# Performance work log

Measured on AMD Instinct MI355X. Metric: run time of the kernel, lower is better.

Reference implementation:

```python
import jax, jax.numpy as jnp
import numpy as np

N = 50000
E = 800000
IN_DIM = 128
LABEL_DIM = 32
D_MODEL = 128
REL_DIM = 32
NUM_LABELS = 1000
REL_BUCKETS = 1024
N_LAYERS = 2
EPS = 1e-5


def setup_inputs() -> dict:
    key = jax.random.key(0)
    ks = jax.random.split(key, 16)
    s = 0.02
    return {
        "x": jax.random.normal(ks[0], (N, IN_DIM), jnp.float32),
        "label": jax.random.randint(ks[1], (N,), 0, NUM_LABELS),
        "edge_index": jax.random.randint(ks[2], (2, E), 0, N),
        "edge_rel": jax.random.randint(ks[3], (E,), 0, REL_BUCKETS),
        "label_emb": jax.random.normal(ks[4], (NUM_LABELS, LABEL_DIM), jnp.float32) * s,
        "in_proj_w": jax.random.normal(ks[5], (IN_DIM + LABEL_DIM, D_MODEL), jnp.float32) * s,
        "in_proj_b": jnp.zeros((D_MODEL,), jnp.float32),
        "rel_emb": jax.random.normal(ks[6], (N_LAYERS, REL_BUCKETS, REL_DIM), jnp.float32) * s,
        "lin_neigh_w": jax.random.normal(ks[7], (N_LAYERS, D_MODEL, D_MODEL), jnp.float32) * s,
        "lin_self_w": jax.random.normal(ks[8], (N_LAYERS, D_MODEL, D_MODEL), jnp.float32) * s,
        "lin_self_b": jnp.zeros((N_LAYERS, D_MODEL), jnp.float32),
        "lin_rel_w": jax.random.normal(ks[9], (N_LAYERS, REL_DIM, D_MODEL), jnp.float32) * s,
        "ln_g": jnp.ones((N_LAYERS, D_MODEL), jnp.float32),
        "ln_b": jnp.zeros((N_LAYERS, D_MODEL), jnp.float32),
    }


def _layernorm(x, g, b):
    mu = jnp.mean(x, axis=-1, keepdims=True)
    var = jnp.mean(jnp.square(x - mu), axis=-1, keepdims=True)
    return (x - mu) * jax.lax.rsqrt(var + EPS) * g + b


def reference(x, label, edge_index, edge_rel, label_emb, in_proj_w, in_proj_b,
              rel_emb, lin_neigh_w, lin_self_w, lin_self_b, lin_rel_w, ln_g, ln_b):
    n = x.shape[0]
    src, dst = edge_index[0], edge_index[1]
    # input projection
    h = jnp.concatenate([x, label_emb[label]], axis=-1) @ in_proj_w + in_proj_b
    h = jax.nn.relu(h)
    # in-degree for mean aggregation (PyG 'mean' gives 0 for isolated nodes)
    deg = jax.ops.segment_sum(jnp.ones((src.shape[0],), h.dtype), dst, num_segments=n)
    inv_deg = jnp.where(deg > 0, 1.0 / jnp.maximum(deg, 1.0), 0.0)[:, None]
    for l in range(N_LAYERS):
        rel = rel_emb[l][edge_rel]                                   # [E, rel_dim]
        msg = h[src] @ lin_neigh_w[l] + rel @ lin_rel_w[l]           # [E, d]
        agg = jax.ops.segment_sum(msg, dst, num_segments=n) * inv_deg
        out = h @ lin_self_w[l] + lin_self_b[l] + agg
        h = _layernorm(jax.nn.relu(out), ln_g[l], ln_b[l])
    return h
```

## Files before the change

### kernel.cpp

```cpp
#include <hip/hip_runtime.h>
#include <hip/hip_bf16.h>

#define N_NODES 50000
#define N_EDGES 800000
#define D 128
#define LABEL_DIM 32
#define REL_DIM 32
#define REL_BUCKETS 1024
#define NUM_LABELS 1000
#define LN_EPS 1e-5f

#define NB 196
#define CAP 6144
#define EPB 1024
#define NE_BLOCKS 782

#define PB_IN 80
#define PB_LEMB 125
#define PB_CAT 144
#define PB_REL 32
#define PREP_UNITS (PB_IN + PB_LEMB + 2 * PB_CAT + 2 * PB_REL)

#define BSTR 144

typedef short bf16x8 __attribute__((ext_vector_type(8)));
typedef float f32x4 __attribute__((ext_vector_type(4)));
typedef float f32x2 __attribute__((ext_vector_type(2)));
typedef unsigned int u32x2 __attribute__((ext_vector_type(2)));
typedef unsigned int u32x4 __attribute__((ext_vector_type(4)));

__device__ inline unsigned short f2bf(float f) {
    __hip_bfloat16 h = __float2bfloat16(f);
    return *reinterpret_cast<unsigned short*>(&h);
}
__device__ inline float bf2f(unsigned short u) {
    return __uint_as_float((unsigned)u << 16);
}

__device__ inline void pack8_fp8(const bf16x8 bv, unsigned& lo, unsigned& hi) {
    float f0 = bf2f((unsigned short)bv[0]), f1 = bf2f((unsigned short)bv[1]);
    float f2 = bf2f((unsigned short)bv[2]), f3 = bf2f((unsigned short)bv[3]);
    float f4 = bf2f((unsigned short)bv[4]), f5 = bf2f((unsigned short)bv[5]);
    float f6 = bf2f((unsigned short)bv[6]), f7 = bf2f((unsigned short)bv[7]);
    lo = __builtin_amdgcn_cvt_pk_fp8_f32(f0, f1, 0u, false);
    lo = __builtin_amdgcn_cvt_pk_fp8_f32(f2, f3, lo, true);
    hi = __builtin_amdgcn_cvt_pk_fp8_f32(f4, f5, 0u, false);
    hi = __builtin_amdgcn_cvt_pk_fp8_f32(f6, f7, hi, true);
}

__global__ __launch_bounds__(256) void scatter_prep_kernel(
    const int* __restrict__ src, const int* __restrict__ dst, const int* __restrict__ rel,
    int* __restrict__ gcur, unsigned* __restrict__ staged_pk, unsigned char* __restrict__ staged_dl,
    const float* __restrict__ in_proj_w, const float* __restrict__ label_emb,
    const float* __restrict__ lin_neigh_w, const float* __restrict__ lin_self_w,
    const float* __restrict__ lin_rel_w, const float* __restrict__ rel_emb,
    unsigned short* __restrict__ Btx, unsigned short* __restrict__ leb,
    unsigned short* __restrict__ Btc0, unsigned short* __restrict__ Btc1,
    unsigned short* __restrict__ relb0, unsigned short* __restrict__ relb1) {
    __shared__ int hist[NB];
    __shared__ int lcur[NB];
    const int t = threadIdx.x;
    const int bid = blockIdx.x;

    if (bid >= NE_BLOCKS) {
        int u = bid - NE_BLOCKS;
        if (u < PB_IN) {
            int idx = u * 256 + t;
            int n = idx / 160, k = idx % 160;
            Btx[idx] = f2bf(in_proj_w[k * 128 + n]);
            return;
        }
        u -= PB_IN;
        if (u < PB_LEMB) {
            int i = u * 256 + t;
            if (i < NUM_LABELS * LABEL_DIM) leb[i] = f2bf(label_emb[i]);
            return;
        }
        u -= PB_LEMB;
        if (u < 2 * PB_CAT) {
            int l = u >= PB_CAT;
            int cb = l ? u - PB_CAT : u;
            int idx = cb * 256 + t;
            int n = idx / 288, k = idx % 288;
            const float* Ws = lin_self_w + (size_t)l * 128 * 128;
            const float* Wn = lin_neigh_w + (size_t)l * 128 * 128;
            const float* Wr = lin_rel_w + (size_t)l * REL_DIM * 128;
            float v = (k < 128) ? Ws[(size_t)k * 128 + n]
                    : (k < 256) ? Wn[(size_t)(k - 128) * 128 + n]
                                : Wr[(size_t)(k - 256) * 128 + n];
            (l ? Btc1 : Btc0)[idx] = f2bf(v);
            return;
        }
        u -= 2 * PB_CAT;
        {
            int l = u >= PB_REL;
            int rb = l ? u - PB_REL : u;
            int idx = rb * 1024 + t * 4;
            float4 v = *(const float4*)(rel_emb + (size_t)l * REL_BUCKETS * REL_DIM + idx);
            unsigned short* out = (l ? relb1 : relb0) + idx;
            out[0] = f2bf(v.x); out[1] = f2bf(v.y);
            out[2] = f2bf(v.z); out[3] = f2bf(v.w);
            return;
        }
    }

    for (int i = t; i < NB; i += 256) hist[i] = 0;
    __syncthreads();
    const int e0 = bid * EPB;
    unsigned char bb[4], dl[4];
#pragma unroll
    for (int i = 0; i < 4; ++i) {
        int e = e0 + i * 256 + t;
        if (e < N_EDGES) {
            int d = dst[e];
            bb[i] = (unsigned char)(d >> 8);
            dl[i] = (unsigned char)(d & 255);
            atomicAdd(&hist[d >> 8], 1);
        }
    }
    __syncthreads();
    for (int b = t; b < NB; b += 256) {
        int hc = hist[b];
        lcur[b] = hc ? (b * CAP + atomicAdd(&gcur[b], hc)) : 0;
    }
    __syncthreads();
#pragma unroll
    for (int i = 0; i < 4; ++i) {
        int e = e0 + i * 256 + t;
        if (e < N_EDGES) {
            int pos = atomicAdd(&lcur[bb[i]], 1);
            staged_pk[pos] = (unsigned)src[e] | ((unsigned)rel[e] << 16);
            staged_dl[pos] = dl[i];
        }
    }
}

__global__ __launch_bounds__(256) void place_in_kernel(
    const int* __restrict__ gcur,
    const unsigned* __restrict__ staged_pk, const unsigned char* __restrict__ staged_dl,
    int* __restrict__ off, int* __restrict__ deg, unsigned* __restrict__ csr_pk,
    const float* __restrict__ X, const unsigned short* __restrict__ Btx,
    const unsigned short* __restrict__ leb, const int* __restrict__ label,
    const float* __restrict__ bias, unsigned short* __restrict__ hb,
    unsigned char* __restrict__ hb8) {
    __shared__ __align__(16) char smem[128 * 160 * 2];
    const int t = threadIdx.x;
    const int bid = blockIdx.x;

    if (bid < NB) {
        int* ph = (int*)smem;
        int* pbuf = ph + 256;
        int* pcur = pbuf + 256;
        const int beg = bid * CAP;
        const int end = beg + gcur[bid];
        ph[t] = 0;
        __syncthreads();
        for (int i = beg + t; i < end; i += 256) atomicAdd(&ph[staged_dl[i]], 1);
        __syncthreads();
        int v = ph[t];
        pbuf[t] = v;
        __syncthreads();
        for (int o = 1; o < 256; o <<= 1) {
            int tv = (t >= o) ? pbuf[t - o] : 0;
            __syncthreads();
            pbuf[t] += tv;
            __syncthreads();
        }
        int node_off = beg + pbuf[t] - v;
        int node = bid * 256 + t;
        if (node < N_NODES) {
            off[node] = node_off;
            deg[node] = v;
        }
        pcur[t] = node_off;
        __syncthreads();
        for (int i = beg + t; i < end; i += 256) {
            int pos = atomicAdd(&pcur[staged_dl[i]], 1);
            csr_pk[pos] = staged_pk[i];
        }
        return;
    }

    unsigned short* sB = (unsigned short*)smem;
    const int mb = bid - NB;
#pragma unroll
    for (int i = 0; i < 10; ++i) {
        int c = t + i * 256;
        int col = c / 20, kch = c % 20;
        int dstc = col * 20 + (kch < 16 ? (kch ^ (col & 7)) : kch);
        *(bf16x8*)&sB[dstc * 8] = *(const bf16x8*)&Btx[c * 8];
    }
    __syncthreads();

    const int wave = t >> 6, lane = t & 63;
    const int m16 = lane & 15, q = lane >> 4;
    const int r0 = mb * 64 + wave * 16;
    const int arow = r0 + m16;
    const bool avalid = arow < N_NODES;
    const float* xp = X + (size_t)(avalid ? arow : 0) * 128 + q * 8;

    f32x4 acc[8];
#pragma unroll
    for (int ct = 0; ct < 8; ++ct) acc[ct] = (f32x4){0.f, 0.f, 0.f, 0.f};

#pragma unroll
    for (int ki = 0; ki < 4; ++ki) {
        bf16x8 af;
        if (avalid) {
            float4 v0 = *(const float4*)(xp + ki * 32);
            float4 v1 = *(const float4*)(xp + ki * 32 + 4);
            af[0] = (short)f2bf(v0.x); af[1] = (short)f2bf(v0.y);
            af[2] = (short)f2bf(v0.z); af[3] = (short)f2bf(v0.w);
            af[4] = (short)f2bf(v1.x); af[5] = (short)f2bf(v1.y);
            af[6] = (short)f2bf(v1.z); af[7] = (short)f2bf(v1.w);
        } else {
            af = (bf16x8){0, 0, 0, 0, 0, 0, 0, 0};
        }
        int kch = ki * 4 + q;
#pragma unroll
        for (int ct = 0; ct < 8; ++ct) {
            int col = ct * 16 + m16;
            int chunk = col * 20 + (kch ^ (m16 & 7));
            bf16x8 bf = *(const bf16x8*)&sB[chunk * 8];
            acc[ct] = __builtin_amdgcn_mfma_f32_16x16x32_bf16(af, bf, acc[ct], 0, 0, 0);
        }
    }
    {
        int lb = avalid ? label[arow] : 0;
        bf16x8 af = *(const bf16x8*)(leb + (size_t)lb * LABEL_DIM + q * 8);
        if (!avalid) af = (bf16x8){0, 0, 0, 0, 0, 0, 0, 0};
        int kch = 16 + q;
#pragma unroll
        for (int ct = 0; ct < 8; ++ct) {
            int col = ct * 16 + m16;
            int chunk = col * 20 + kch;
            bf16x8 bf = *(const bf16x8*)&sB[chunk * 8];
            acc[ct] = __builtin_amdgcn_mfma_f32_16x16x32_bf16(af, bf, acc[ct], 0, 0, 0);
        }
    }

    unsigned short hbv[8][4];
#pragma unroll
    for (int ct = 0; ct < 8; ++ct) {
        int colg = ct * 16 + m16;
        float bs = bias[colg];
#pragma unroll
        for (int r = 0; r < 4; ++r) {
            int row = r0 + q * 4 + r;
            float v = fmaxf(acc[ct][r] + bs, 0.f);
            hbv[ct][r] = f2bf(v);
            if (row < N_NODES) hb[(size_t)row * 128 + colg] = hbv[ct][r];
        }
    }

    __syncthreads();
    unsigned short* bounce = sB;
#pragma unroll
    for (int ct = 0; ct < 8; ++ct) {
        int colg = ct * 16 + m16;
#pragma unroll
        for (int r = 0; r < 4; ++r)
            bounce[(wave * 16 + q * 4 + r) * BSTR + colg] = hbv[ct][r];
    }
    __syncthreads();
    {
        int rl = t >> 2;
        int grow = mb * 64 + rl;
        if (grow < N_NODES) {
            const unsigned short* bp = bounce + rl * BSTR + (t & 3) * 32;
            unsigned o[8];
#pragma unroll
            for (int k = 0; k < 4; ++k) {
                bf16x8 bv = *(const bf16x8*)(bp + k * 8);
                pack8_fp8(bv, o[2 * k], o[2 * k + 1]);
            }
            u32x4* dp = (u32x4*)(hb8 + (size_t)grow * 128 + (t & 3) * 32);
            dp[0] = (u32x4){o[0], o[1], o[2], o[3]};
            dp[1] = (u32x4){o[4], o[5], o[6], o[7]};
        }
    }
}

__global__ __launch_bounds__(256) void agg_raw_kernel(const unsigned char* __restrict__ hb8,
                                                      const unsigned short* __restrict__ relb,
                                                      const int* __restrict__ off,
                                                      const int* __restrict__ deg,
                                                      const unsigned* __restrict__ csr_pk,
                                                      unsigned short* __restrict__ Sm,
                                                      unsigned short* __restrict__ Rm) {
    const int wave = threadIdx.x >> 6;
    const int lane = threadIdx.x & 63;
    const int node = blockIdx.x * 4 + wave;
    if (node >= N_NODES) return;
    const int q = lane >> 4, l16 = lane & 15;
    const int beg = off[node];
    const int dcnt = deg[node];
    const int co = l16 * 8;

    float acc[8];
    float ra0 = 0.f, ra1 = 0.f;
#pragma unroll
    for (int j = 0; j < 8; ++j) acc[j] = 0.f;

    unsigned pkv = 0;
    if (lane < dcnt) pkv = csr_pk[beg + lane];

    const int dcl = dcnt < 64 ? dcnt : 64;
    for (int s = 0; s < dcl; s += 16) {
        unsigned pkk[4];
        float mk[4];
#pragma unroll
        for (int k = 0; k < 4; ++k) {
            int slot = s + k * 4 + q;
            pkk[k] = (unsigned)__shfl((int)pkv, slot);
            mk[k] = (slot < dcnt) ? 1.f : 0.f;
        }
#pragma unroll
        for (int k = 0; k < 4; ++k) {
            u32x2 hv = *(const u32x2*)(hb8 + ((size_t)(pkk[k] & 0xffffu) << 7) + co);
            unsigned rw = *(const unsigned*)(relb + ((size_t)(pkk[k] >> 16) << 5) + l16 * 2);
            float m = mk[k];
            f32x2 d0 = __builtin_amdgcn_cvt_pk_f32_fp8(hv[0], false);
            f32x2 d1 = __builtin_amdgcn_cvt_pk_f32_fp8(hv[0], true);
            f32x2 d2 = __builtin_amdgcn_cvt_pk_f32_fp8(hv[1], false);
            f32x2 d3 = __builtin_amdgcn_cvt_pk_f32_fp8(hv[1], true);
            acc[0] = fmaf(m, d0[0], acc[0]); acc[1] = fmaf(m, d0[1], acc[1]);
            acc[2] = fmaf(m, d1[0], acc[2]); acc[3] = fmaf(m, d1[1], acc[3]);
            acc[4] = fmaf(m, d2[0], acc[4]); acc[5] = fmaf(m, d2[1], acc[5]);
            acc[6] = fmaf(m, d3[0], acc[6]); acc[7] = fmaf(m, d3[1], acc[7]);
            ra0 = fmaf(m, bf2f((unsigned short)(rw & 0xffffu)), ra0);
            ra1 = fmaf(m, bf2f((unsigned short)(rw >> 16)), ra1);
        }
    }

    const int end = beg + dcnt;
    for (int e = beg + 64; e < end; e += 8) {
        int i0 = e + q, i1 = e + 4 + q;
        float m0 = 1.f, m1 = 1.f;
        if (i0 >= end) { i0 = beg; m0 = 0.f; }
        if (i1 >= end) { i1 = beg; m1 = 0.f; }
        unsigned pk0 = csr_pk[i0];
        unsigned pk1 = csr_pk[i1];
        u32x2 hv0 = *(const u32x2*)(hb8 + ((size_t)(pk0 & 0xffffu) << 7) + co);
        u32x2 hv1 = *(const u32x2*)(hb8 + ((size_t)(pk1 & 0xffffu) << 7) + co);
        unsigned rw0 = *(const unsigned*)(relb + ((size_t)(pk0 >> 16) << 5) + l16 * 2);
        unsigned rw1 = *(const unsigned*)(relb + ((size_t)(pk1 >> 16) << 5) + l16 * 2);
        {
            f32x2 d0 = __builtin_amdgcn_cvt_pk_f32_fp8(hv0[0], false);
            f32x2 d1 = __builtin_amdgcn_cvt_pk_f32_fp8(hv0[0], true);
            f32x2 d2 = __builtin_amdgcn_cvt_pk_f32_fp8(hv0[1], false);
            f32x2 d3 = __builtin_amdgcn_cvt_pk_f32_fp8(hv0[1], true);
            acc[0] = fmaf(m0, d0[0], acc[0]); acc[1] = fmaf(m0, d0[1], acc[1]);
            acc[2] = fmaf(m0, d1[0], acc[2]); acc[3] = fmaf(m0, d1[1], acc[3]);
            acc[4] = fmaf(m0, d2[0], acc[4]); acc[5] = fmaf(m0, d2[1], acc[5]);
            acc[6] = fmaf(m0, d3[0], acc[6]); acc[7] = fmaf(m0, d3[1], acc[7]);
        }
        {
            f32x2 d0 = __builtin_amdgcn_cvt_pk_f32_fp8(hv1[0], false);
            f32x2 d1 = __builtin_amdgcn_cvt_pk_f32_fp8(hv1[0], true);
            f32x2 d2 = __builtin_amdgcn_cvt_pk_f32_fp8(hv1[1], false);
            f32x2 d3 = __builtin_amdgcn_cvt_pk_f32_fp8(hv1[1], true);
            acc[0] = fmaf(m1, d0[0], acc[0]); acc[1] = fmaf(m1, d0[1], acc[1]);
            acc[2] = fmaf(m1, d1[0], acc[2]); acc[3] = fmaf(m1, d1[1], acc[3]);
            acc[4] = fmaf(m1, d2[0], acc[4]); acc[5] = fmaf(m1, d2[1], acc[5]);
            acc[6] = fmaf(m1, d3[0], acc[6]); acc[7] = fmaf(m1, d3[1], acc[7]);
        }
        ra0 = fmaf(m0, bf2f((unsigned short)(rw0 & 0xffffu)), ra0);
        ra1 = fmaf(m0, bf2f((unsigned short)(rw0 >> 16)), ra1);
        ra0 = fmaf(m1, bf2f((unsigned short)(rw1 & 0xffffu)), ra0);
        ra1 = fmaf(m1, bf2f((unsigned short)(rw1 >> 16)), ra1);
    }

#pragma unroll
    for (int j = 0; j < 8; ++j) {
        acc[j] += __shfl_xor(acc[j], 16);
        acc[j] += __shfl_xor(acc[j], 32);
    }
    ra0 += __shfl_xor(ra0, 16); ra0 += __shfl_xor(ra0, 32);
    ra1 += __shfl_xor(ra1, 16); ra1 += __shfl_xor(ra1, 32);

    float inv = (dcnt > 0) ? 1.f / (float)dcnt : 0.f;
    if (q == 0) {
        bf16x8 ob;
#pragma unroll
        for (int j = 0; j < 8; ++j) ob[j] = (short)f2bf(acc[j] * inv);
        *(bf16x8*)(Sm + ((size_t)node << 7) + co) = ob;
        unsigned pk = (unsigned)f2bf(ra0 * inv) | ((unsigned)f2bf(ra1 * inv) << 16);
        ((unsigned*)(Rm + ((size_t)node << 5)))[l16] = pk;
    }
}

template <bool LAST>
__global__ __launch_bounds__(256) void gemm_ln_kernel(const unsigned short* __restrict__ Btc,
                                                      unsigned short* __restrict__ hb,
                                                      unsigned char* __restrict__ hb8,
                                                      const unsigned short* __restrict__ Sm,
                                                      const unsigned short* __restrict__ Rm,
                                                      const float* __restrict__ bias,
                                                      const float* __restrict__ g,
                                                      const float* __restrict__ b,
                                                      float* __restrict__ hout) {
    __shared__ unsigned short sB[128 * 36 * 8];
    const int t = threadIdx.x;
#pragma unroll
    for (int i = 0; i < 18; ++i) {
        int c = t + i * 256;
        int col = c / 36, kch = c % 36;
        int swz = (kch < 32) ? (kch ^ (col & 7)) : (32 + ((kch - 32) ^ (col & 3)));
        *(bf16x8*)&sB[(col * 36 + swz) * 8] = *(const bf16x8*)&Btc[c * 8];
    }
    __syncthreads();

    const int wave = t >> 6, lane = t & 63;
    const int m16 = lane & 15, q = lane >> 4;
    const int r0 = blockIdx.x * 64 + wave * 16;
    const int arow = r0 + m16;
    const bool avalid = arow < N_NODES;
    const int sr = avalid ? arow : 0;
    const unsigned short* hp = hb + (size_t)sr * 128 + q * 8;
    const unsigned short* sp = Sm + (size_t)sr * 128 + q * 8;
    const unsigned short* rp = Rm + (size_t)sr * 32 + q * 8;

    f32x4 acc[8];
#pragma unroll
    for (int ct = 0; ct < 8; ++ct) acc[ct] = (f32x4){0.f, 0.f, 0.f, 0.f};
    const bf16x8 zf = (bf16x8){0, 0, 0, 0, 0, 0, 0, 0};

#pragma unroll
    for (int ki = 0; ki < 4; ++ki) {
        bf16x8 af = *(const bf16x8*)(hp + ki * 32);
        if (!avalid) af = zf;
        int kch = ki * 4 + q;
#pragma unroll
        for (int ct = 0; ct < 8; ++ct) {
            int col = ct * 16 + m16;
            bf16x8 bf = *(const bf16x8*)&sB[(col * 36 + (kch ^ (m16 & 7))) * 8];
            acc[ct] = __builtin_amdgcn_mfma_f32_16x16x32_bf16(af, bf, acc[ct], 0, 0, 0);
        }
    }
#pragma unroll
    for (int ki = 0; ki < 4; ++ki) {
        bf16x8 af = *(const bf16x8*)(sp + ki * 32);
        if (!avalid) af = zf;
        int kch = 16 + ki * 4 + q;
#pragma unroll
        for (int ct = 0; ct < 8; ++ct) {
            int col = ct * 16 + m16;
            bf16x8 bf = *(const bf16x8*)&sB[(col * 36 + (kch ^ (m16 & 7))) * 8];
            acc[ct] = __builtin_amdgcn_mfma_f32_16x16x32_bf16(af, bf, acc[ct], 0, 0, 0);
        }
    }
    {
        bf16x8 af = *(const bf16x8*)rp;
        if (!avalid) af = zf;
#pragma unroll
        for (int ct = 0; ct < 8; ++ct) {
            int col = ct * 16 + m16;
            bf16x8 bf = *(const bf16x8*)&sB[(col * 36 + 32 + (q ^ (m16 & 3))) * 8];
            acc[ct] = __builtin_amdgcn_mfma_f32_16x16x32_bf16(af, bf, acc[ct], 0, 0, 0);
        }
    }

    float bs[8], gs[8], bbs[8];
#pragma unroll
    for (int ct = 0; ct < 8; ++ct) {
        int cg2 = ct * 16 + m16;
        bs[ct] = bias[cg2];
        gs[ct] = g[cg2];
        bbs[ct] = b[cg2];
    }
    unsigned short hbv[4][8];
#pragma unroll
    for (int r = 0; r < 4; ++r) {
        int row = r0 + q * 4 + r;
        float v[8];
        float s = 0.f;
#pragma unroll
        for (int ct = 0; ct < 8; ++ct) {
            float val = fmaxf(acc[ct][r] + bs[ct], 0.f);
            v[ct] = val;
            s += val;
        }
#pragma unroll
        for (int o = 8; o > 0; o >>= 1) s += __shfl_xor(s, o);
        float mu = s * (1.f / 128.f);
        float qs = 0.f;
#pragma unroll
        for (int ct = 0; ct < 8; ++ct) {
            float dd = v[ct] - mu;
            v[ct] = dd;
            qs += dd * dd;
        }
#pragma unroll
        for (int o = 8; o > 0; o >>= 1) qs += __shfl_xor(qs, o);
        float rstd = rsqrtf(qs * (1.f / 128.f) + LN_EPS);
#pragma unroll
        for (int ct = 0; ct < 8; ++ct) {
            int colg = ct * 16 + m16;
            float o2 = v[ct] * rstd * gs[ct] + bbs[ct];
            hbv[r][ct] = f2bf(o2);
            if (row < N_NODES) {
                if constexpr (LAST) {
                    hout[(size_t)row * 128 + colg] = o2;
                } else {
                    hb[(size_t)row * 128 + colg] = hbv[r][ct];
                }
            }
        }
    }

    if constexpr (!LAST) {
        __syncthreads();
        unsigned short* bounce = sB;
#pragma unroll
        for (int r = 0; r < 4; ++r) {
            int rl = wave * 16 + q * 4 + r;
#pragma unroll
            for (int ct = 0; ct < 8; ++ct)
                bounce[rl * BSTR + ct * 16 + m16] = hbv[r][ct];
        }
        __syncthreads();
        int rl = t >> 2;
        int grow = blockIdx.x * 64 + rl;
        if (grow < N_NODES) {
            const unsigned short* bp = bounce + rl * BSTR + (t & 3) * 32;
            unsigned o[8];
#pragma unroll
            for (int k = 0; k < 4; ++k) {
                bf16x8 bv = *(const bf16x8*)(bp + k * 8);
                pack8_fp8(bv, o[2 * k], o[2 * k + 1]);
            }
            u32x4* dp = (u32x4*)(hb8 + (size_t)grow * 128 + (t & 3) * 32);
            dp[0] = (u32x4){o[0], o[1], o[2], o[3]};
            dp[1] = (u32x4){o[4], o[5], o[6], o[7]};
        }
    }
}


extern "C" void kernel_launch(void* const* d_in, const int* in_sizes, int n_in,
                              void* d_out, int out_size, void* d_ws, size_t ws_size,
                              hipStream_t stream) {
    const float* x          = (const float*)d_in[0];
    const int*   label      = (const int*)d_in[1];
    const int*   edge_index = (const int*)d_in[2];
    const int*   edge_rel   = (const int*)d_in[3];
    const float* label_emb  = (const float*)d_in[4];
    const float* in_proj_w  = (const float*)d_in[5];
    const float* in_proj_b  = (const float*)d_in[6];
    const float* rel_emb    = (const float*)d_in[7];
    const float* lin_neigh_w = (const float*)d_in[8];
    const float* lin_self_w  = (const float*)d_in[9];
    const float* lin_self_b  = (const float*)d_in[10];
    const float* lin_rel_w   = (const float*)d_in[11];
    const float* ln_g        = (const float*)d_in[12];
    const float* ln_b        = (const float*)d_in[13];
    float* h = (float*)d_out;

    char* p = (char*)d_ws;
    auto alloc = [&](size_t bytes) {
        char* r = p;
        p += (bytes + 255) & ~(size_t)255;
        return r;
    };
    int* gcur        = (int*)alloc((size_t)NB * 4);
    int* off         = (int*)alloc((size_t)N_NODES * 4);
    int* deg         = (int*)alloc((size_t)N_NODES * 4);
    unsigned* csr_pk = (unsigned*)alloc((size_t)NB * CAP * 4);
    unsigned* staged_pk = (unsigned*)alloc((size_t)NB * CAP * 4);
    unsigned char* staged_dl = (unsigned char*)alloc((size_t)NB * CAP);
    unsigned short* hb  = (unsigned short*)alloc((size_t)N_NODES * 128 * 2);
    unsigned char*  hb8 = (unsigned char*)alloc((size_t)N_NODES * 128);
    unsigned short* Sm  = (unsigned short*)alloc((size_t)N_NODES * 128 * 2);
    unsigned short* Rm  = (unsigned short*)alloc((size_t)N_NODES * 32 * 2);
    unsigned short* Btx = (unsigned short*)alloc((size_t)128 * 160 * 2);
    unsigned short* leb = (unsigned short*)alloc((size_t)NUM_LABELS * LABEL_DIM * 2);
    unsigned short* Btc0 = (unsigned short*)alloc((size_t)128 * 288 * 2);
    unsigned short* Btc1 = (unsigned short*)alloc((size_t)128 * 288 * 2);
    unsigned short* relb0 = (unsigned short*)alloc((size_t)REL_BUCKETS * REL_DIM * 2);
    unsigned short* relb1 = (unsigned short*)alloc((size_t)REL_BUCKETS * REL_DIM * 2);

    const int* src = edge_index;
    const int* dst = edge_index + N_EDGES;

    hipMemsetAsync(gcur, 0, (size_t)NB * 4, stream);

    scatter_prep_kernel<<<NE_BLOCKS + PREP_UNITS, 256, 0, stream>>>(
        src, dst, edge_rel, gcur, staged_pk, staged_dl,
        in_proj_w, label_emb, lin_neigh_w, lin_self_w, lin_rel_w, rel_emb,
        Btx, leb, Btc0, Btc1, relb0, relb1);

    place_in_kernel<<<NB + NE_BLOCKS, 256, 0, stream>>>(
        gcur, staged_pk, staged_dl, off, deg, csr_pk,
        x, Btx, leb, label, in_proj_b, hb, hb8);

    const int gemm_grid = (N_NODES + 63) / 64;
    const int agg_grid = (N_NODES + 3) / 4;

    agg_raw_kernel<<<agg_grid, 256, 0, stream>>>(
        hb8, relb0, off, deg, csr_pk, Sm, Rm);
    gemm_ln_kernel<false><<<gemm_grid, 256, 0, stream>>>(
        Btc0, hb, hb8, Sm, Rm, lin_self_b, ln_g, ln_b, nullptr);
    agg_raw_kernel<<<agg_grid, 256, 0, stream>>>(
        hb8, relb1, off, deg, csr_pk, Sm, Rm);
    gemm_ln_kernel<true><<<gemm_grid, 256, 0, stream>>>(
        Btc1, hb, hb8, Sm, Rm, lin_self_b + 128, ln_g + 128, ln_b + 128, h);
}
```

Before: 240.4 us.

## Use fixed-capacity per-node edge slots and fuse aggregation into the layer GEMM

```diff
diff --git a/kernel.cpp b/kernel.cpp
--- a/kernel.cpp
+++ b/kernel.cpp
@@ -10,16 +10,17 @@
 #define NUM_LABELS 1000
 #define LN_EPS 1e-5f
 
-#define NB 196
-#define CAP 6144
+#define CAPN 64
 #define EPB 1024
 #define NE_BLOCKS 782
+#define GEMM_BLOCKS 782
 
 #define PB_IN 80
 #define PB_LEMB 125
 #define PB_CAT 144
 #define PB_REL 32
-#define PREP_UNITS (PB_IN + PB_LEMB + 2 * PB_CAT + 2 * PB_REL)
+#define PB_ZERO 49
+#define PREP_GRID (PB_IN + PB_LEMB + 2 * PB_CAT + 2 * PB_REL + PB_ZERO)
 
 #define BSTR 144
 
@@ -48,97 +49,64 @@
     hi = __builtin_amdgcn_cvt_pk_fp8_f32(f6, f7, hi, true);
 }
 
-__global__ __launch_bounds__(256) void scatter_prep_kernel(
-    const int* __restrict__ src, const int* __restrict__ dst, const int* __restrict__ rel,
-    int* __restrict__ gcur, unsigned* __restrict__ staged_pk, unsigned char* __restrict__ staged_dl,
+__global__ __launch_bounds__(256) void prep_zero_kernel(
     const float* __restrict__ in_proj_w, const float* __restrict__ label_emb,
     const float* __restrict__ lin_neigh_w, const float* __restrict__ lin_self_w,
     const float* __restrict__ lin_rel_w, const float* __restrict__ rel_emb,
     unsigned short* __restrict__ Btx, unsigned short* __restrict__ leb,
     unsigned short* __restrict__ Btc0, unsigned short* __restrict__ Btc1,
-    unsigned short* __restrict__ relb0, unsigned short* __restrict__ relb1) {
-    __shared__ int hist[NB];
-    __shared__ int lcur[NB];
+    unsigned short* __restrict__ relb0, unsigned short* __restrict__ relb1,
+    int* __restrict__ dcnt) {
+    int u = blockIdx.x;
     const int t = threadIdx.x;
-    const int bid = blockIdx.x;
-
-    if (bid >= NE_BLOCKS) {
-        int u = bid - NE_BLOCKS;
-        if (u < PB_IN) {
-            int idx = u * 256 + t;
-            int n = idx / 160, k = idx % 160;
-            Btx[idx] = f2bf(in_proj_w[k * 128 + n]);
-            return;
-        }
-        u -= PB_IN;
-        if (u < PB_LEMB) {
-            int i = u * 256 + t;
-            if (i < NUM_LABELS * LABEL_DIM) leb[i] = f2bf(label_emb[i]);
-            return;
-        }
-        u -= PB_LEMB;
-        if (u < 2 * PB_CAT) {
-            int l = u >= PB_CAT;
-            int cb = l ? u - PB_CAT : u;
-            int idx = cb * 256 + t;
-            int n = idx / 288, k = idx % 288;
-            const float* Ws = lin_self_w + (size_t)l * 128 * 128;
-            const float* Wn = lin_neigh_w + (size_t)l * 128 * 128;
-            const float* Wr = lin_rel_w + (size_t)l * REL_DIM * 128;
-            float v = (k < 128) ? Ws[(size_t)k * 128 + n]
-                    : (k < 256) ? Wn[(size_t)(k - 128) * 128 + n]
-                                : Wr[(size_t)(k - 256) * 128 + n];
-            (l ? Btc1 : Btc0)[idx] = f2bf(v);
-            return;
-        }
-        u -= 2 * PB_CAT;
-        {
-            int l = u >= PB_REL;
-            int rb = l ? u - PB_REL : u;
-            int idx = rb * 1024 + t * 4;
-            float4 v = *(const float4*)(rel_emb + (size_t)l * REL_BUCKETS * REL_DIM + idx);
-            unsigned short* out = (l ? relb1 : relb0) + idx;
-            out[0] = f2bf(v.x); out[1] = f2bf(v.y);
-            out[2] = f2bf(v.z); out[3] = f2bf(v.w);
-            return;
-        }
-    }
-
-    for (int i = t; i < NB; i += 256) hist[i] = 0;
-    __syncthreads();
-    const int e0 = bid * EPB;
-    unsigned char bb[4], dl[4];
-#pragma unroll
-    for (int i = 0; i < 4; ++i) {
-        int e = e0 + i * 256 + t;
-        if (e < N_EDGES) {
-            int d = dst[e];
-            bb[i] = (unsigned char)(d >> 8);
-            dl[i] = (unsigned char)(d & 255);
-            atomicAdd(&hist[d >> 8], 1);
-        }
-    }
-    __syncthreads();
-    for (int b = t; b < NB; b += 256) {
-        int hc = hist[b];
-        lcur[b] = hc ? (b * CAP + atomicAdd(&gcur[b], hc)) : 0;
-    }
-    __syncthreads();
-#pragma unroll
-    for (int i = 0; i < 4; ++i) {
-        int e = e0 + i * 256 + t;
-        if (e < N_EDGES) {
-            int pos = atomicAdd(&lcur[bb[i]], 1);
-            staged_pk[pos] = (unsigned)src[e] | ((unsigned)rel[e] << 16);
-            staged_dl[pos] = dl[i];
-        }
-    }
-}
-
-__global__ __launch_bounds__(256) void place_in_kernel(
-    const int* __restrict__ gcur,
-    const unsigned* __restrict__ staged_pk, const unsigned char* __restrict__ staged_dl,
-    int* __restrict__ off, int* __restrict__ deg, unsigned* __restrict__ csr_pk,
+    if (u < PB_IN) {
+        int idx = u * 256 + t;
+        int n = idx / 160, k = idx % 160;
+        Btx[idx] = f2bf(in_proj_w[k * 128 + n]);
+        return;
+    }
+    u -= PB_IN;
+    if (u < PB_LEMB) {
+        int i = u * 256 + t;
+        if (i < NUM_LABELS * LABEL_DIM) leb[i] = f2bf(label_emb[i]);
+        return;
+    }
+    u -= PB_LEMB;
+    if (u < 2 * PB_CAT) {
+        int l = u >= PB_CAT;
+        int cb = l ? u - PB_CAT : u;
+        int idx = cb * 256 + t;
+        int n = idx / 288, k = idx % 288;
+        const float* Ws = lin_self_w + (size_t)l * 128 * 128;
+        const float* Wn = lin_neigh_w + (size_t)l * 128 * 128;
+        const float* Wr = lin_rel_w + (size_t)l * REL_DIM * 128;
+        float v = (k < 128) ? Ws[(size_t)k * 128 + n]
+                : (k < 256) ? Wn[(size_t)(k - 128) * 128 + n]
+                            : Wr[(size_t)(k - 256) * 128 + n];
+        (l ? Btc1 : Btc0)[idx] = f2bf(v);
+        return;
+    }
+    u -= 2 * PB_CAT;
+    if (u < 2 * PB_REL) {
+        int l = u >= PB_REL;
+        int rb = l ? u - PB_REL : u;
+        int idx = rb * 1024 + t * 4;
+        float4 v = *(const float4*)(rel_emb + (size_t)l * REL_BUCKETS * REL_DIM + idx);
+        unsigned short* out = (l ? relb1 : relb0) + idx;
+        out[0] = f2bf(v.x); out[1] = f2bf(v.y);
+        out[2] = f2bf(v.z); out[3] = f2bf(v.w);
+        return;
+    }
+    u -= 2 * PB_REL;
+    {
+        int idx4 = u * 256 + t;
+        if (idx4 < N_NODES / 4) ((int4*)dcnt)[idx4] = make_int4(0, 0, 0, 0);
+    }
+}
+
+__global__ __launch_bounds__(256) void bin_in_kernel(
+    const int* __restrict__ src, const int* __restrict__ dst, const int* __restrict__ rel,
+    int* __restrict__ dcnt, unsigned* __restrict__ csr_pk,
     const float* __restrict__ X, const unsigned short* __restrict__ Btx,
     const unsigned short* __restrict__ leb, const int* __restrict__ label,
     const float* __restrict__ bias, unsigned short* __restrict__ hb,
@@ -147,42 +115,24 @@
     const int t = threadIdx.x;
     const int bid = blockIdx.x;
 
-    if (bid < NB) {
-        int* ph = (int*)smem;
-        int* pbuf = ph + 256;
-        int* pcur = pbuf + 256;
-        const int beg = bid * CAP;
-        const int end = beg + gcur[bid];
-        ph[t] = 0;
-        __syncthreads();
-        for (int i = beg + t; i < end; i += 256) atomicAdd(&ph[staged_dl[i]], 1);
-        __syncthreads();
-        int v = ph[t];
-        pbuf[t] = v;
-        __syncthreads();
-        for (int o = 1; o < 256; o <<= 1) {
-            int tv = (t >= o) ? pbuf[t - o] : 0;
-            __syncthreads();
-            pbuf[t] += tv;
-            __syncthreads();
-        }
-        int node_off = beg + pbuf[t] - v;
-        int node = bid * 256 + t;
-        if (node < N_NODES) {
-            off[node] = node_off;
-            deg[node] = v;
-        }
-        pcur[t] = node_off;
-        __syncthreads();
-        for (int i = beg + t; i < end; i += 256) {
-            int pos = atomicAdd(&pcur[staged_dl[i]], 1);
-            csr_pk[pos] = staged_pk[i];
+    if (bid < NE_BLOCKS) {
+        const int e0 = bid * EPB;
+#pragma unroll
+        for (int i = 0; i < 4; ++i) {
+            int e = e0 + i * 256 + t;
+            if (e < N_EDGES) {
+                int d = dst[e];
+                int slot = atomicAdd(&dcnt[d], 1);
+                if (slot < CAPN)
+                    csr_pk[(size_t)d * CAPN + slot] =
+                        (unsigned)src[e] | ((unsigned)rel[e] << 16);
+            }
         }
         return;
     }
 
     unsigned short* sB = (unsigned short*)smem;
-    const int mb = bid - NB;
+    const int mb = bid - NE_BLOCKS;
 #pragma unroll
     for (int i = 0; i < 10; ++i) {
         int c = t + i * 256;
@@ -281,182 +231,165 @@
     }
 }
 
-__global__ __launch_bounds__(256) void agg_raw_kernel(const unsigned char* __restrict__ hb8,
-                                                      const unsigned short* __restrict__ relb,
-                                                      const int* __restrict__ off,
-                                                      const int* __restrict__ deg,
-                                                      const unsigned* __restrict__ csr_pk,
-                                                      unsigned short* __restrict__ Sm,
-                                                      unsigned short* __restrict__ Rm) {
-    const int wave = threadIdx.x >> 6;
-    const int lane = threadIdx.x & 63;
-    const int node = blockIdx.x * 4 + wave;
-    if (node >= N_NODES) return;
-    const int q = lane >> 4, l16 = lane & 15;
-    const int beg = off[node];
-    const int dcnt = deg[node];
-    const int co = l16 * 8;
-
-    float acc[8];
-    float ra0 = 0.f, ra1 = 0.f;
-#pragma unroll
-    for (int j = 0; j < 8; ++j) acc[j] = 0.f;
-
-    unsigned pkv = 0;
-    if (lane < dcnt) pkv = csr_pk[beg + lane];
-
-    const int dcl = dcnt < 64 ? dcnt : 64;
-    for (int s = 0; s < dcl; s += 16) {
-        unsigned pkk[4];
-        float mk[4];
-#pragma unroll
-        for (int k = 0; k < 4; ++k) {
-            int slot = s + k * 4 + q;
-            pkk[k] = (unsigned)__shfl((int)pkv, slot);
-            mk[k] = (slot < dcnt) ? 1.f : 0.f;
-        }
-#pragma unroll
-        for (int k = 0; k < 4; ++k) {
-            u32x2 hv = *(const u32x2*)(hb8 + ((size_t)(pkk[k] & 0xffffu) << 7) + co);
-            unsigned rw = *(const unsigned*)(relb + ((size_t)(pkk[k] >> 16) << 5) + l16 * 2);
-            float m = mk[k];
-            f32x2 d0 = __builtin_amdgcn_cvt_pk_f32_fp8(hv[0], false);
-            f32x2 d1 = __builtin_amdgcn_cvt_pk_f32_fp8(hv[0], true);
-            f32x2 d2 = __builtin_amdgcn_cvt_pk_f32_fp8(hv[1], false);
-            f32x2 d3 = __builtin_amdgcn_cvt_pk_f32_fp8(hv[1], true);
-            acc[0] = fmaf(m, d0[0], acc[0]); acc[1] = fmaf(m, d0[1], acc[1]);
-            acc[2] = fmaf(m, d1[0], acc[2]); acc[3] = fmaf(m, d1[1], acc[3]);
-            acc[4] = fmaf(m, d2[0], acc[4]); acc[5] = fmaf(m, d2[1], acc[5]);
-            acc[6] = fmaf(m, d3[0], acc[6]); acc[7] = fmaf(m, d3[1], acc[7]);
-            ra0 = fmaf(m, bf2f((unsigned short)(rw & 0xffffu)), ra0);
-            ra1 = fmaf(m, bf2f((unsigned short)(rw >> 16)), ra1);
-        }
-    }
-
-    const int end = beg + dcnt;
-    for (int e = beg + 64; e < end; e += 8) {
-        int i0 = e + q, i1 = e + 4 + q;
-        float m0 = 1.f, m1 = 1.f;
-        if (i0 >= end) { i0 = beg; m0 = 0.f; }
-        if (i1 >= end) { i1 = beg; m1 = 0.f; }
-        unsigned pk0 = csr_pk[i0];
-        unsigned pk1 = csr_pk[i1];
-        u32x2 hv0 = *(const u32x2*)(hb8 + ((size_t)(pk0 & 0xffffu) << 7) + co);
-        u32x2 hv1 = *(const u32x2*)(hb8 + ((size_t)(pk1 & 0xffffu) << 7) + co);
-        unsigned rw0 = *(const unsigned*)(relb + ((size_t)(pk0 >> 16) << 5) + l16 * 2);
-        unsigned rw1 = *(const unsigned*)(relb + ((size_t)(pk1 >> 16) << 5) + l16 * 2);
-        {
-            f32x2 d0 = __builtin_amdgcn_cvt_pk_f32_fp8(hv0[0], false);
-            f32x2 d1 = __builtin_amdgcn_cvt_pk_f32_fp8(hv0[0], true);
-            f32x2 d2 = __builtin_amdgcn_cvt_pk_f32_fp8(hv0[1], false);
-            f32x2 d3 = __builtin_amdgcn_cvt_pk_f32_fp8(hv0[1], true);
-            acc[0] = fmaf(m0, d0[0], acc[0]); acc[1] = fmaf(m0, d0[1], acc[1]);
-            acc[2] = fmaf(m0, d1[0], acc[2]); acc[3] = fmaf(m0, d1[1], acc[3]);
-            acc[4] = fmaf(m0, d2[0], acc[4]); acc[5] = fmaf(m0, d2[1], acc[5]);
-            acc[6] = fmaf(m0, d3[0], acc[6]); acc[7] = fmaf(m0, d3[1], acc[7]);
-        }
-        {
-            f32x2 d0 = __builtin_amdgcn_cvt_pk_f32_fp8(hv1[0], false);
-            f32x2 d1 = __builtin_amdgcn_cvt_pk_f32_fp8(hv1[0], true);
-            f32x2 d2 = __builtin_amdgcn_cvt_pk_f32_fp8(hv1[1], false);
-            f32x2 d3 = __builtin_amdgcn_cvt_pk_f32_fp8(hv1[1], true);
-            acc[0] = fmaf(m1, d0[0], acc[0]); acc[1] = fmaf(m1, d0[1], acc[1]);
-            acc[2] = fmaf(m1, d1[0], acc[2]); acc[3] = fmaf(m1, d1[1], acc[3]);
-            acc[4] = fmaf(m1, d2[0], acc[4]); acc[5] = fmaf(m1, d2[1], acc[5]);
-            acc[6] = fmaf(m1, d3[0], acc[6]); acc[7] = fmaf(m1, d3[1], acc[7]);
-        }
-        ra0 = fmaf(m0, bf2f((unsigned short)(rw0 & 0xffffu)), ra0);
-        ra1 = fmaf(m0, bf2f((unsigned short)(rw0 >> 16)), ra1);
-        ra0 = fmaf(m1, bf2f((unsigned short)(rw1 & 0xffffu)), ra0);
-        ra1 = fmaf(m1, bf2f((unsigned short)(rw1 >> 16)), ra1);
-    }
-
-#pragma unroll
-    for (int j = 0; j < 8; ++j) {
-        acc[j] += __shfl_xor(acc[j], 16);
-        acc[j] += __shfl_xor(acc[j], 32);
-    }
-    ra0 += __shfl_xor(ra0, 16); ra0 += __shfl_xor(ra0, 32);
-    ra1 += __shfl_xor(ra1, 16); ra1 += __shfl_xor(ra1, 32);
-
-    float inv = (dcnt > 0) ? 1.f / (float)dcnt : 0.f;
-    if (q == 0) {
-        bf16x8 ob;
-#pragma unroll
-        for (int j = 0; j < 8; ++j) ob[j] = (short)f2bf(acc[j] * inv);
-        *(bf16x8*)(Sm + ((size_t)node << 7) + co) = ob;
-        unsigned pk = (unsigned)f2bf(ra0 * inv) | ((unsigned)f2bf(ra1 * inv) << 16);
-        ((unsigned*)(Rm + ((size_t)node << 5)))[l16] = pk;
-    }
-}
-
 template <bool LAST>
-__global__ __launch_bounds__(256) void gemm_ln_kernel(const unsigned short* __restrict__ Btc,
-                                                      unsigned short* __restrict__ hb,
-                                                      unsigned char* __restrict__ hb8,
-                                                      const unsigned short* __restrict__ Sm,
-                                                      const unsigned short* __restrict__ Rm,
-                                                      const float* __restrict__ bias,
-                                                      const float* __restrict__ g,
-                                                      const float* __restrict__ b,
-                                                      float* __restrict__ hout) {
-    __shared__ unsigned short sB[128 * 36 * 8];
+__global__ __launch_bounds__(256) void layer_kernel(
+    const unsigned short* __restrict__ Btc,
+    unsigned short* __restrict__ hb,
+    const unsigned char* __restrict__ hb8_in,
+    unsigned char* __restrict__ hb8_out,
+    const unsigned short* __restrict__ relb,
+    const int* __restrict__ dcnt, const unsigned* __restrict__ csr_pk,
+    const float* __restrict__ bias, const float* __restrict__ g,
+    const float* __restrict__ b, float* __restrict__ hout) {
+    __shared__ __align__(16) unsigned short sB[128 * 20 * 8];
+    __shared__ __align__(16) unsigned short sm_s[64 * 128];
+    __shared__ __align__(16) unsigned rm_s[64 * 16];
+
     const int t = threadIdx.x;
-#pragma unroll
-    for (int i = 0; i < 18; ++i) {
-        int c = t + i * 256;
-        int col = c / 36, kch = c % 36;
-        int swz = (kch < 32) ? (kch ^ (col & 7)) : (32 + ((kch - 32) ^ (col & 3)));
-        *(bf16x8*)&sB[(col * 36 + swz) * 8] = *(const bf16x8*)&Btc[c * 8];
-    }
-    __syncthreads();
-
     const int wave = t >> 6, lane = t & 63;
     const int m16 = lane & 15, q = lane >> 4;
-    const int r0 = blockIdx.x * 64 + wave * 16;
-    const int arow = r0 + m16;
+    const int r0 = blockIdx.x * 64;
+    const int arow = r0 + wave * 16 + m16;
     const bool avalid = arow < N_NODES;
     const int sr = avalid ? arow : 0;
-    const unsigned short* hp = hb + (size_t)sr * 128 + q * 8;
-    const unsigned short* sp = Sm + (size_t)sr * 128 + q * 8;
-    const unsigned short* rp = Rm + (size_t)sr * 32 + q * 8;
+
+    bf16x8 aself[4];
+    {
+        const unsigned short* hp = hb + (size_t)sr * 128 + q * 8;
+        const bf16x8 zf = (bf16x8){0, 0, 0, 0, 0, 0, 0, 0};
+#pragma unroll
+        for (int ki = 0; ki < 4; ++ki) {
+            bf16x8 af = *(const bf16x8*)(hp + ki * 32);
+            aself[ki] = avalid ? af : zf;
+        }
+    }
+
+#pragma unroll
+    for (int i = 0; i < 8; ++i) {
+        int c = t + i * 256;
+        int col = c >> 4, kc = c & 15;
+        *(bf16x8*)&sB[(col * 16 + (kc ^ (col & 7))) * 8] = *(const bf16x8*)&Btc[(col * 36 + kc) * 8];
+    }
+    __syncthreads();
+
+    {
+        const int node_base = r0 + wave * 16;
+        const int l16 = m16;
+        const int co = l16 * 8;
+        int dcv = 0;
+        {
+            int nb = node_base + lane;
+            if (lane < 16 && nb < N_NODES) dcv = dcnt[nb];
+        }
+        int dc_next = __shfl(dcv, 0);
+        dc_next = dc_next < CAPN ? dc_next : CAPN;
+        unsigned pk_cur = 0;
+        if (lane < dc_next) pk_cur = csr_pk[(size_t)node_base * CAPN + lane];
+
+        for (int i = 0; i < 16; ++i) {
+            const int dc = dc_next;
+            const int dtrue = __shfl(dcv, i);
+            unsigned pk_next = 0;
+            if (i < 15) {
+                dc_next = __shfl(dcv, i + 1);
+                dc_next = dc_next < CAPN ? dc_next : CAPN;
+                if (lane < dc_next) pk_next = csr_pk[(size_t)(node_base + i + 1) * CAPN + lane];
+            }
+            float acc[8];
+#pragma unroll
+            for (int j = 0; j < 8; ++j) acc[j] = 0.f;
+            float ra0 = 0.f, ra1 = 0.f;
+
+            for (int s = 0; s < dc; s += 16) {
+                unsigned pkk[4];
+                float mk[4];
+#pragma unroll
+                for (int k = 0; k < 4; ++k) {
+                    int slot = s + k * 4 + q;
+                    pkk[k] = (unsigned)__shfl((int)pk_cur, slot);
+                    mk[k] = (slot < dc) ? 1.f : 0.f;
+                }
+#pragma unroll
+                for (int k = 0; k < 4; ++k) {
+                    u32x2 hv = *(const u32x2*)(hb8_in + ((size_t)(pkk[k] & 0xffffu) << 7) + co);
+                    unsigned rw = *(const unsigned*)(relb + ((size_t)(pkk[k] >> 16) << 5) + l16 * 2);
+                    float m = mk[k];
+                    f32x2 d0 = __builtin_amdgcn_cvt_pk_f32_fp8(hv[0], false);
+                    f32x2 d1 = __builtin_amdgcn_cvt_pk_f32_fp8(hv[0], true);
+                    f32x2 d2 = __builtin_amdgcn_cvt_pk_f32_fp8(hv[1], false);
+                    f32x2 d3 = __builtin_amdgcn_cvt_pk_f32_fp8(hv[1], true);
+                    acc[0] = fmaf(m, d0[0], acc[0]); acc[1] = fmaf(m, d0[1], acc[1]);
+                    acc[2] = fmaf(m, d1[0], acc[2]); acc[3] = fmaf(m, d1[1], acc[3]);
+                    acc[4] = fmaf(m, d2[0], acc[4]); acc[5] = fmaf(m, d2[1], acc[5]);
+                    acc[6] = fmaf(m, d3[0], acc[6]); acc[7] = fmaf(m, d3[1], acc[7]);
+                    ra0 = fmaf(m, bf2f((unsigned short)(rw & 0xffffu)), ra0);
+                    ra1 = fmaf(m, bf2f((unsigned short)(rw >> 16)), ra1);
+                }
+            }
+#pragma unroll
+            for (int j = 0; j < 8; ++j) {
+                acc[j] += __shfl_xor(acc[j], 16);
+                acc[j] += __shfl_xor(acc[j], 32);
+            }
+            ra0 += __shfl_xor(ra0, 16); ra0 += __shfl_xor(ra0, 32);
+            ra1 += __shfl_xor(ra1, 16); ra1 += __shfl_xor(ra1, 32);
+
+            if (q == 0) {
+                float inv = (dtrue > 0) ? 1.f / (float)dtrue : 0.f;
+                bf16x8 ob;
+#pragma unroll
+                for (int j = 0; j < 8; ++j) ob[j] = (short)f2bf(acc[j] * inv);
+                int row = wave * 16 + i;
+                *(bf16x8*)&sm_s[(row * 16 + (l16 ^ (row & 7))) * 8] = ob;
+                rm_s[row * 16 + (l16 ^ ((row & 3) << 2))] =
+                    (unsigned)f2bf(ra0 * inv) | ((unsigned)f2bf(ra1 * inv) << 16);
+            }
+            pk_cur = pk_next;
+        }
+    }
 
     f32x4 acc[8];
 #pragma unroll
     for (int ct = 0; ct < 8; ++ct) acc[ct] = (f32x4){0.f, 0.f, 0.f, 0.f};
-    const bf16x8 zf = (bf16x8){0, 0, 0, 0, 0, 0, 0, 0};
-
 #pragma unroll
     for (int ki = 0; ki < 4; ++ki) {
-        bf16x8 af = *(const bf16x8*)(hp + ki * 32);
-        if (!avalid) af = zf;
         int kch = ki * 4 + q;
 #pragma unroll
         for (int ct = 0; ct < 8; ++ct) {
             int col = ct * 16 + m16;
-            bf16x8 bf = *(const bf16x8*)&sB[(col * 36 + (kch ^ (m16 & 7))) * 8];
+            bf16x8 bf = *(const bf16x8*)&sB[(col * 16 + (kch ^ (m16 & 7))) * 8];
+            acc[ct] = __builtin_amdgcn_mfma_f32_16x16x32_bf16(aself[ki], bf, acc[ct], 0, 0, 0);
+        }
+    }
+    __syncthreads();
+
+#pragma unroll
+    for (int i = 0; i < 10; ++i) {
+        int c = t + i * 256;
+        int col = c / 20, j = c % 20;
+        int swz = (j < 16) ? (j ^ (col & 7)) : (16 + ((j - 16) ^ (col & 3)));
+        *(bf16x8*)&sB[(col * 20 + swz) * 8] = *(const bf16x8*)&Btc[(col * 36 + 16 + j) * 8];
+    }
+    __syncthreads();
+
+    const int lr = wave * 16 + m16;
+#pragma unroll
+    for (int ki = 0; ki < 4; ++ki) {
+        int kch = ki * 4 + q;
+        bf16x8 af = *(const bf16x8*)&sm_s[(lr * 16 + (kch ^ (m16 & 7))) * 8];
+#pragma unroll
+        for (int ct = 0; ct < 8; ++ct) {
+            int col = ct * 16 + m16;
+            bf16x8 bf = *(const bf16x8*)&sB[(col * 20 + (kch ^ (m16 & 7))) * 8];
             acc[ct] = __builtin_amdgcn_mfma_f32_16x16x32_bf16(af, bf, acc[ct], 0, 0, 0);
         }
     }
-#pragma unroll
-    for (int ki = 0; ki < 4; ++ki) {
-        bf16x8 af = *(const bf16x8*)(sp + ki * 32);
-        if (!avalid) af = zf;
-        int kch = 16 + ki * 4 + q;
+    {
+        bf16x8 af = *(const bf16x8*)&rm_s[lr * 16 + ((q * 4) ^ ((m16 & 3) << 2))];
 #pragma unroll
         for (int ct = 0; ct < 8; ++ct) {
             int col = ct * 16 + m16;
-            bf16x8 bf = *(const bf16x8*)&sB[(col * 36 + (kch ^ (m16 & 7))) * 8];
-            acc[ct] = __builtin_amdgcn_mfma_f32_16x16x32_bf16(af, bf, acc[ct], 0, 0, 0);
-        }
-    }
-    {
-        bf16x8 af = *(const bf16x8*)rp;
-        if (!avalid) af = zf;
-#pragma unroll
-        for (int ct = 0; ct < 8; ++ct) {
-            int col = ct * 16 + m16;
-            bf16x8 bf = *(const bf16x8*)&sB[(col * 36 + 32 + (q ^ (m16 & 3))) * 8];
+            bf16x8 bf = *(const bf16x8*)&sB[(col * 20 + 16 + (q ^ (m16 & 3))) * 8];
             acc[ct] = __builtin_amdgcn_mfma_f32_16x16x32_bf16(af, bf, acc[ct], 0, 0, 0);
         }
     }
@@ -469,10 +402,11 @@
         gs[ct] = g[cg2];
         bbs[ct] = b[cg2];
     }
+    const int rw0 = r0 + wave * 16;
     unsigned short hbv[4][8];
 #pragma unroll
     for (int r = 0; r < 4; ++r) {
-        int row = r0 + q * 4 + r;
+        int row = rw0 + q * 4 + r;
         float v[8];
         float s = 0.f;
 #pragma unroll
@@ -521,7 +455,7 @@
         }
         __syncthreads();
         int rl = t >> 2;
-        int grow = blockIdx.x * 64 + rl;
+        int grow = r0 + rl;
         if (grow < N_NODES) {
             const unsigned short* bp = bounce + rl * BSTR + (t & 3) * 32;
             unsigned o[8];
@@ -530,7 +464,7 @@
                 bf16x8 bv = *(const bf16x8*)(bp + k * 8);
                 pack8_fp8(bv, o[2 * k], o[2 * k + 1]);
             }
-            u32x4* dp = (u32x4*)(hb8 + (size_t)grow * 128 + (t & 3) * 32);
+            u32x4* dp = (u32x4*)(hb8_out + (size_t)grow * 128 + (t & 3) * 32);
             dp[0] = (u32x4){o[0], o[1], o[2], o[3]};
             dp[1] = (u32x4){o[4], o[5], o[6], o[7]};
         }
@@ -563,18 +497,13 @@
         p += (bytes + 255) & ~(size_t)255;
         return r;
     };
-    int* gcur        = (int*)alloc((size_t)NB * 4);
-    int* off         = (int*)alloc((size_t)N_NODES * 4);
-    int* deg         = (int*)alloc((size_t)N_NODES * 4);
-    unsigned* csr_pk = (unsigned*)alloc((size_t)NB * CAP * 4);
-    unsigned* staged_pk = (unsigned*)alloc((size_t)NB * CAP * 4);
-    unsigned char* staged_dl = (unsigned char*)alloc((size_t)NB * CAP);
-    unsigned short* hb  = (unsigned short*)alloc((size_t)N_NODES * 128 * 2);
-    unsigned char*  hb8 = (unsigned char*)alloc((size_t)N_NODES * 128);
-    unsigned short* Sm  = (unsigned short*)alloc((size_t)N_NODES * 128 * 2);
-    unsigned short* Rm  = (unsigned short*)alloc((size_t)N_NODES * 32 * 2);
-    unsigned short* Btx = (unsigned short*)alloc((size_t)128 * 160 * 2);
-    unsigned short* leb = (unsigned short*)alloc((size_t)NUM_LABELS * LABEL_DIM * 2);
+    int* dcnt        = (int*)alloc((size_t)N_NODES * 4);
+    unsigned* csr_pk = (unsigned*)alloc((size_t)N_NODES * CAPN * 4);
+    unsigned short* hb   = (unsigned short*)alloc((size_t)N_NODES * 128 * 2);
+    unsigned char*  hb8a = (unsigned char*)alloc((size_t)N_NODES * 128);
+    unsigned char*  hb8b = (unsigned char*)alloc((size_t)N_NODES * 128);
+    unsigned short* Btx  = (unsigned short*)alloc((size_t)128 * 160 * 2);
+    unsigned short* leb  = (unsigned short*)alloc((size_t)NUM_LABELS * LABEL_DIM * 2);
     unsigned short* Btc0 = (unsigned short*)alloc((size_t)128 * 288 * 2);
     unsigned short* Btc1 = (unsigned short*)alloc((size_t)128 * 288 * 2);
     unsigned short* relb0 = (unsigned short*)alloc((size_t)REL_BUCKETS * REL_DIM * 2);
@@ -583,26 +512,19 @@
     const int* src = edge_index;
     const int* dst = edge_index + N_EDGES;
 
-    hipMemsetAsync(gcur, 0, (size_t)NB * 4, stream);
-
-    scatter_prep_kernel<<<NE_BLOCKS + PREP_UNITS, 256, 0, stream>>>(
-        src, dst, edge_rel, gcur, staged_pk, staged_dl,
+    prep_zero_kernel<<<PREP_GRID, 256, 0, stream>>>(
         in_proj_w, label_emb, lin_neigh_w, lin_self_w, lin_rel_w, rel_emb,
-        Btx, leb, Btc0, Btc1, relb0, relb1);
-
-    place_in_kernel<<<NB + NE_BLOCKS, 256, 0, stream>>>(
-        gcur, staged_pk, staged_dl, off, deg, csr_pk,
-        x, Btx, leb, label, in_proj_b, hb, hb8);
-
-    const int gemm_grid = (N_NODES + 63) / 64;
-    const int agg_grid = (N_NODES + 3) / 4;
-
-    agg_raw_kernel<<<agg_grid, 256, 0, stream>>>(
-        hb8, relb0, off, deg, csr_pk, Sm, Rm);
-    gemm_ln_kernel<false><<<gemm_grid, 256, 0, stream>>>(
-        Btc0, hb, hb8, Sm, Rm, lin_self_b, ln_g, ln_b, nullptr);
-    agg_raw_kernel<<<agg_grid, 256, 0, stream>>>(
-        hb8, relb1, off, deg, csr_pk, Sm, Rm);
-    gemm_ln_kernel<true><<<gemm_grid, 256, 0, stream>>>(
-        Btc1, hb, hb8, Sm, Rm, lin_self_b + 128, ln_g + 128, ln_b + 128, h);
-}
+        Btx, leb, Btc0, Btc1, relb0, relb1, dcnt);
+
+    bin_in_kernel<<<NE_BLOCKS + GEMM_BLOCKS, 256, 0, stream>>>(
+        src, dst, edge_rel, dcnt, csr_pk,
+        x, Btx, leb, label, in_proj_b, hb, hb8a);
+
+    layer_kernel<false><<<GEMM_BLOCKS, 256, 0, stream>>>(
+        Btc0, hb, hb8a, hb8b, relb0, dcnt, csr_pk,
+        lin_self_b, ln_g, ln_b, nullptr);
+
+    layer_kernel<true><<<GEMM_BLOCKS, 256, 0, stream>>>(
+        Btc1, hb, hb8b, nullptr, relb1, dcnt, csr_pk,
+        lin_self_b + 128, ln_g + 128, ln_b + 128, h);
+}
```

Measured after the change: 284.9 us. 18.5% more time.
